# Performance work log

Hardware: AMD Instinct MI355X
Metric: run time of the kernel (lower is better)

Reference implementation:

```python
import jax, jax.numpy as jnp
import numpy as np

N, D_IN, D_HID, D_CODE, K = 131072, 768, 512, 256, 512

def setup_inputs() -> dict:
    key = jax.random.key(0)
    ks = jax.random.split(key, 10)
    s1 = 1.0 / np.sqrt(D_IN); s2 = 1.0 / np.sqrt(D_HID); s3 = 1.0 / np.sqrt(D_CODE)
    return {
        "x": jax.random.normal(ks[0], (N, D_IN), jnp.float32),
        "W1": jax.random.normal(ks[1], (D_IN, D_HID), jnp.float32) * s1,
        "b1": jnp.zeros((D_HID,), jnp.float32),
        "W2": jax.random.normal(ks[2], (D_HID, D_CODE), jnp.float32) * s2,
        "b2": jnp.zeros((D_CODE,), jnp.float32),
        "codebook": jax.random.normal(ks[3], (K, D_CODE), jnp.float32),
        "W3": jax.random.normal(ks[4], (D_CODE, D_HID), jnp.float32) * s3,
        "b3": jnp.zeros((D_HID,), jnp.float32),
        "W4": jax.random.normal(ks[5], (D_HID, D_IN), jnp.float32) * s2,
        "b4": jnp.zeros((D_IN,), jnp.float32),
    }

def reference(x, W1, b1, W2, b2, codebook, W3, b3, W4, b4):
    # encoder: Linear -> ReLU -> Linear
    z = jax.nn.relu(x @ W1 + b1) @ W2 + b2                      # [N, D_CODE]
    # nearest-code search: squared euclidean distances to codebook
    # ||z||^2 - 2 z.c + ||c||^2  (||z||^2 constant per row, drop for argmin)
    dots = z @ codebook.T                                        # [N, K]
    dist = jnp.sum(codebook * codebook, axis=-1)[None, :] - 2.0 * dots
    indices = jnp.argmin(dist, axis=-1)                          # [N] int
    quantized = codebook[indices]                                # gather [N, D_CODE]
    # commitment loss: mse(quantize.detach(), z) * commitment_weight(=1.0)
    commit_loss = jnp.mean((jax.lax.stop_gradient(quantized) - z) ** 2)
    # straight-through estimator
    quantized_st = z + jax.lax.stop_gradient(quantized - z)
    # decoder: Linear -> ReLU -> Linear
    recon = jax.nn.relu(quantized_st @ W3 + b3) @ W4 + b4        # [N, D_IN]
    return recon, indices.astype(jnp.int32), commit_loss
```

## Files before the change

kernel.cpp:

```cpp
#include <hip/hip_runtime.h>
#include <hip/hip_bf16.h>
#include <math.h>

#define N_ROWS 131072
#define DIN    768
#define DHID   512
#define DCODE  256
#define KC     512
#define NFUSE  768
#define TAU1   0.6f
#define TAU2   5e-3f
#define CAP    16384

typedef short short8 __attribute__((ext_vector_type(8)));
typedef float f32x4  __attribute__((ext_vector_type(4)));
typedef unsigned int   u32;
typedef unsigned short u16;

__device__ __forceinline__ void gload16(const void* g, void* l) {
    __builtin_amdgcn_global_load_lds(
        (const __attribute__((address_space(1))) u32*)g,
        (__attribute__((address_space(3))) u32*)l, 16, 0, 0);
}

__device__ __forceinline__ u16 f2bf(float f) {
    u32 u = __builtin_bit_cast(u32, f);
    return (u16)((u + 0x7fffu + ((u >> 16) & 1u)) >> 16);
}
__device__ __forceinline__ float bf2f(u16 h) {
    u32 u = ((u32)h) << 16;
    return __builtin_bit_cast(float, u);
}

__device__ __forceinline__ void xcd_swizzle(int& bxs, int& bys) {
    const int GX  = gridDim.x;
    const int nwg = GX * gridDim.y;
    const int lid = blockIdx.y * GX + blockIdx.x;
    const int chunk = nwg >> 3;
    const int nlid  = (lid & 7) * chunk + (lid >> 3);
    bxs = nlid % GX;
    bys = nlid / GX;
}

__device__ __forceinline__ void split_write(char* hidst, char* lodst, float4 v) {
    u16 h0 = f2bf(v.x), h1 = f2bf(v.y), h2 = f2bf(v.z), h3 = f2bf(v.w);
    u16 l0 = f2bf(__fsub_rn(v.x, bf2f(h0)));
    u16 l1 = f2bf(__fsub_rn(v.y, bf2f(h1)));
    u16 l2 = f2bf(__fsub_rn(v.z, bf2f(h2)));
    u16 l3 = f2bf(__fsub_rn(v.w, bf2f(h3)));
    ushort4 hi; hi.x = h0; hi.y = h1; hi.z = h2; hi.w = h3;
    ushort4 lo; lo.x = l0; lo.y = l1; lo.z = l2; lo.w = l3;
    *(ushort4*)hidst = hi;
    *(ushort4*)lodst = lo;
}

template<int EPI>
__global__ __launch_bounds__(256, 3)
void split2_gemm(const float* __restrict__ Af32,
                 const u16* __restrict__ Ahi, const u16* __restrict__ Alo,
                 const u16* __restrict__ Bhi, const u16* __restrict__ Blo,
                 const float* __restrict__ bias,
                 const float* __restrict__ cnorm,
                 u16* __restrict__ Chi, u16* __restrict__ Clo,
                 float* __restrict__ pd1, int* __restrict__ pi1,
                 float* __restrict__ pd2,
                 int M, int N, int K)
{
    __shared__ char lds[32768];
    const int t = threadIdx.x, lane = t & 63, wid = t >> 6;
    const int wm = wid >> 1, wn = wid & 1;
    int bxs, bys; xcd_swizzle(bxs, bys);
    const int bm = bys * 128, bn = bxs * 128;

    const int sr = lane >> 3, qq = lane & 7, sl = qq ^ sr;
    const u16* bsrc[4];
    #pragma unroll
    for (int c = 0; c < 4; c++) {
        int row = bn + (wid * 4 + c) * 8 + sr;
        const u16* base = (sl < 4) ? Bhi : Blo;
        bsrc[c] = base + (size_t)row * K + (sl & 3) * 8;
    }
    const u16* asrc[4];
    const float* a32src[4];
    int adhi[4], adlo[4];
    if constexpr (EPI == 1) {
        #pragma unroll
        for (int c = 0; c < 4; c++) {
            int row = bm + (wid * 4 + c) * 8 + sr;
            const u16* base = (sl < 4) ? Ahi : Alo;
            asrc[c] = base + (size_t)row * K + (sl & 3) * 8;
        }
    } else {
        #pragma unroll
        for (int c = 0; c < 4; c++) {
            int id = c * 256 + t;
            int row = id >> 3, k4 = id & 7;
            a32src[c] = Af32 + (size_t)(bm + row) * K + k4 * 4;
            int s = k4 >> 1, hf = k4 & 1;
            adhi[c] = row * 128 + ((s ^ (row & 7)) << 4) + hf * 8;
            adlo[c] = row * 128 + (((s | 4) ^ (row & 7)) << 4) + hf * 8;
        }
    }

    f32x4 acc[4][4];
    #pragma unroll
    for (int i = 0; i < 4; i++)
        #pragma unroll
        for (int j = 0; j < 4; j++) acc[i][j] = (f32x4)0.f;

    const int fr = lane & 15, sw = lane & 7;
    const int offhi = (((lane >> 4) ^ sw) << 4);
    const int offlo = ((((lane >> 4) | 4) ^ sw) << 4);
    const int arow = wm * 64 + fr, brow = wn * 64 + fr;
    const int NT = K >> 5;

    for (int tt = 0; tt < NT; tt++) {
        __syncthreads();
        const int kadv = tt * 32;
        #pragma unroll
        for (int c = 0; c < 4; c++)
            gload16(bsrc[c] + kadv, lds + 16384 + (wid * 4 + c) * 1024);
        if constexpr (EPI == 1) {
            #pragma unroll
            for (int c = 0; c < 4; c++)
                gload16(asrc[c] + kadv, lds + (wid * 4 + c) * 1024);
        } else {
            #pragma unroll
            for (int c = 0; c < 4; c++) {
                float4 v = *(const float4*)(a32src[c] + kadv);
                split_write(lds + adhi[c], lds + adlo[c], v);
            }
        }
        __syncthreads();
        char* ab  = lds;
        char* bb2 = lds + 16384;
        short8 ah[4], al[4];
        #pragma unroll
        for (int i = 0; i < 4; i++) {
            ah[i] = *(const short8*)(ab + ((arow + i * 16) << 7) + offhi);
            al[i] = *(const short8*)(ab + ((arow + i * 16) << 7) + offlo);
        }
        #pragma unroll
        for (int j = 0; j < 4; j++) {
            short8 bh = *(const short8*)(bb2 + ((brow + j * 16) << 7) + offhi);
            short8 bl = *(const short8*)(bb2 + ((brow + j * 16) << 7) + offlo);
            #pragma unroll
            for (int i = 0; i < 4; i++) {
                acc[i][j] = __builtin_amdgcn_mfma_f32_16x16x32_bf16(ah[i], bh, acc[i][j], 0, 0, 0);
                acc[i][j] = __builtin_amdgcn_mfma_f32_16x16x32_bf16(al[i], bh, acc[i][j], 0, 0, 0);
                acc[i][j] = __builtin_amdgcn_mfma_f32_16x16x32_bf16(ah[i], bl, acc[i][j], 0, 0, 0);
            }
        }
    }

    if constexpr (EPI == 1) {
        const int ec = lane & 15, g = lane >> 4;
        float cnv[4], bcv[4];
        #pragma unroll
        for (int j = 0; j < 4; j++) {
            int c = bn + wn * 64 + j * 16 + ec;
            cnv[j] = cnorm[c]; bcv[j] = bias[c];
        }
        const int strip = bxs * 2 + wn;
        #pragma unroll
        for (int i = 0; i < 4; i++) {
            #pragma unroll
            for (int e = 0; e < 4; e++) {
                float d1 = INFINITY, d2 = INFINITY; int i1 = 0x7fffffff;
                #pragma unroll
                for (int j = 0; j < 4; j++) {
                    int c = bn + wn * 64 + j * 16 + ec;
                    float d = __fsub_rn(cnv[j],
                              __fmul_rn(2.0f, __fadd_rn(acc[i][j][e], bcv[j])));
                    if (d < d1 || (d == d1 && c < i1)) { d2 = d1; d1 = d; i1 = c; }
                    else if (d < d2) d2 = d;
                }
                #pragma unroll
                for (int m = 1; m < 16; m <<= 1) {
                    float od1 = __shfl_xor(d1, m);
                    int   oi1 = __shfl_xor(i1, m);
                    float od2 = __shfl_xor(d2, m);
                    if (od1 < d1 || (od1 == d1 && oi1 < i1)) {
                        d2 = fminf(d1, od2); d1 = od1; i1 = oi1;
                    } else d2 = fminf(d2, od1);
                }
                if (ec == 0) {
                    int r = bm + wm * 64 + i * 16 + g * 4 + e;
                    pd1[(size_t)strip * M + r] = d1;
                    pi1[(size_t)strip * M + r] = i1;
                    pd2[(size_t)strip * M + r] = d2;
                }
            }
        }
        return;
    } else {
        const int er = (lane >> 4) * 4, ec = lane & 15;
        #pragma unroll
        for (int j = 0; j < 4; j++) {
            int col = bn + wn * 64 + j * 16 + ec;
            float bb = bias[col];
            #pragma unroll
            for (int i = 0; i < 4; i++) {
                #pragma unroll
                for (int e = 0; e < 4; e++) {
                    int r = bm + wm * 64 + i * 16 + er + e;
                    float v = fmaxf(__fadd_rn(acc[i][j][e], bb), 0.f);
                    u16 hi = f2bf(v);
                    u16 lo = f2bf(__fsub_rn(v, bf2f(hi)));
                    Chi[(size_t)r * N + col] = hi;
                    Clo[(size_t)r * N + col] = lo;
                }
            }
        }
    }
}

__global__ __launch_bounds__(256, 3)
void dots_gemm(const u16* __restrict__ A, const u16* __restrict__ BT,
               const float* __restrict__ bias, const float* __restrict__ cnorm,
               float* __restrict__ pd1, int* __restrict__ pi1,
               float* __restrict__ pd2, float* __restrict__ pzn,
               int M, int N, int K)
{
    __shared__ char lds[32768];
    const int t = threadIdx.x, lane = t & 63, wid = t >> 6;
    const int wm = wid >> 1, wn = wid & 1;
    int bxs, bys; xcd_swizzle(bxs, bys);
    const int bm = bys * 128, bn = bxs * 128;

    const int sr = lane >> 3;
    const int sc = ((lane & 7) ^ sr) * 8;
    const u16* aptr[4];
    const u16* bptr[4];
    #pragma unroll
    for (int c = 0; c < 4; c++) {
        int gc = wid * 4 + c;
        aptr[c] = A  + (size_t)(bm + 8 * gc + sr) * K + sc;
        bptr[c] = BT + (size_t)(bn + 8 * gc + sr) * K + sc;
    }

    f32x4 acc[4][4];
    #pragma unroll
    for (int i = 0; i < 4; i++)
        #pragma unroll
        for (int j = 0; j < 4; j++) acc[i][j] = (f32x4)0.f;

    const int koff0 = (16 * (lane >> 4))      ^ ((lane & 7) << 4);
    const int koff1 = (64 + 16 * (lane >> 4)) ^ ((lane & 7) << 4);
    const int arow_rd = wm * 64 + (lane & 15);
    const int brow_rd = wn * 64 + (lane & 15);

    const int NT = K >> 6;
    for (int tt = 0; tt < NT; tt++) {
        __syncthreads();
        const int k0 = tt << 6;
        #pragma unroll
        for (int c = 0; c < 4; c++) {
            int gc = wid * 4 + c;
            gload16(aptr[c] + k0, lds + gc * 1024);
            gload16(bptr[c] + k0, lds + 16384 + gc * 1024);
        }
        __syncthreads();
        char* ldsA = lds;
        char* ldsB = lds + 16384;
        #pragma unroll
        for (int kk = 0; kk < 2; kk++) {
            const int ko = kk ? koff1 : koff0;
            short8 af[4], bfr[4];
            #pragma unroll
            for (int i = 0; i < 4; i++)
                af[i]  = *(const short8*)(ldsA + (arow_rd + i * 16) * 128 + ko);
            #pragma unroll
            for (int j = 0; j < 4; j++)
                bfr[j] = *(const short8*)(ldsB + (brow_rd + j * 16) * 128 + ko);
            #pragma unroll
            for (int i = 0; i < 4; i++)
                #pragma unroll
                for (int j = 0; j < 4; j++)
                    acc[i][j] = __builtin_amdgcn_mfma_f32_16x16x32_bf16(
                        af[i], bfr[j], acc[i][j], 0, 0, 0);
        }
    }

    const int ec = lane & 15, g = lane >> 4;
    if (bxs < 4) {
        float cnv[4], bcv[4];
        #pragma unroll
        for (int j = 0; j < 4; j++) {
            int c = bn + wn * 64 + j * 16 + ec;
            cnv[j] = cnorm[c]; bcv[j] = bias[c];
        }
        const int strip = bxs * 2 + wn;
        #pragma unroll
        for (int i = 0; i < 4; i++) {
            #pragma unroll
            for (int e = 0; e < 4; e++) {
                float d1 = INFINITY, d2 = INFINITY; int i1 = 0x7fffffff;
                #pragma unroll
                for (int j = 0; j < 4; j++) {
                    int c = bn + wn * 64 + j * 16 + ec;
                    float d = __fsub_rn(cnv[j],
                              __fmul_rn(2.0f, __fadd_rn(acc[i][j][e], bcv[j])));
                    if (d < d1 || (d == d1 && c < i1)) { d2 = d1; d1 = d; i1 = c; }
                    else if (d < d2) d2 = d;
                }
                #pragma unroll
                for (int m = 1; m < 16; m <<= 1) {
                    float od1 = __shfl_xor(d1, m);
                    int   oi1 = __shfl_xor(i1, m);
                    float od2 = __shfl_xor(d2, m);
                    if (od1 < d1 || (od1 == d1 && oi1 < i1)) {
                        d2 = fminf(d1, od2); d1 = od1; i1 = oi1;
                    } else d2 = fminf(d2, od1);
                }
                if (ec == 0) {
                    int r = bm + wm * 64 + i * 16 + g * 4 + e;
                    pd1[(size_t)strip * M + r] = d1;
                    pi1[(size_t)strip * M + r] = i1;
                    pd2[(size_t)strip * M + r] = d2;
                }
            }
        }
    } else {
        float bcv[4];
        #pragma unroll
        for (int j = 0; j < 4; j++)
            bcv[j] = bias[bn + wn * 64 + j * 16 + ec];
        const int zs = (bxs - 4) * 2 + wn;
        #pragma unroll
        for (int i = 0; i < 4; i++) {
            #pragma unroll
            for (int e = 0; e < 4; e++) {
                float s = 0.f;
                #pragma unroll
                for (int j = 0; j < 4; j++) {
                    float zv = acc[i][j][e] + bcv[j];
                    s = fmaf(zv, zv, s);
                }
                #pragma unroll
                for (int m = 1; m < 16; m <<= 1) s += __shfl_xor(s, m);
                if (ec == 0) {
                    int r = bm + wm * 64 + i * 16 + g * 4 + e;
                    pzn[(size_t)zs * M + r] = s;
                }
            }
        }
    }
}

template<bool RELU, bool OUT_BF16>
__global__ __launch_bounds__(256, 3)
void mfma_gemm(const u16* __restrict__ A, const u16* __restrict__ BT,
               const float* __restrict__ bias,
               void* __restrict__ Cout, int M, int N, int K)
{
    __shared__ char lds[32768];
    const int t    = threadIdx.x;
    const int lane = t & 63, wid = t >> 6;
    const int wm   = wid >> 1, wn = wid & 1;
    int bxs, bys;
    xcd_swizzle(bxs, bys);
    const int bm = bys * 128, bn = bxs * 128;

    const int sr = lane >> 3;
    const int sc = ((lane & 7) ^ sr) * 8;
    const u16* aptr[4];
    const u16* bptr[4];
    #pragma unroll
    for (int c = 0; c < 4; c++) {
        int gc   = wid * 4 + c;
        aptr[c] = A  + (size_t)(bm + 8 * gc + sr) * K + sc;
        bptr[c] = BT + (size_t)(bn + 8 * gc + sr) * K + sc;
    }

    f32x4 acc[4][4];
    #pragma unroll
    for (int i = 0; i < 4; i++)
        #pragma unroll
        for (int j = 0; j < 4; j++) acc[i][j] = (f32x4)0.f;

    const int koff0 = (16 * (lane >> 4))      ^ ((lane & 7) << 4);
    const int koff1 = (64 + 16 * (lane >> 4)) ^ ((lane & 7) << 4);
    const int arow_rd = wm * 64 + (lane & 15);
    const int brow_rd = wn * 64 + (lane & 15);

    const int NT = K >> 6;
    for (int tt = 0; tt < NT; tt++) {
        __syncthreads();
        const int k0 = tt << 6;
        #pragma unroll
        for (int c = 0; c < 4; c++) {
            int gc = wid * 4 + c;
            gload16(aptr[c] + k0, lds + gc * 1024);
            gload16(bptr[c] + k0, lds + 16384 + gc * 1024);
        }
        __syncthreads();
        char* ldsA = lds;
        char* ldsB = lds + 16384;
        #pragma unroll
        for (int kk = 0; kk < 2; kk++) {
            const int ko = kk ? koff1 : koff0;
            short8 af[4], bfr[4];
            #pragma unroll
            for (int i = 0; i < 4; i++)
                af[i]  = *(const short8*)(ldsA + (arow_rd + i * 16) * 128 + ko);
            #pragma unroll
            for (int j = 0; j < 4; j++)
                bfr[j] = *(const short8*)(ldsB + (brow_rd + j * 16) * 128 + ko);
            #pragma unroll
            for (int i = 0; i < 4; i++)
                #pragma unroll
                for (int j = 0; j < 4; j++)
                    acc[i][j] = __builtin_amdgcn_mfma_f32_16x16x32_bf16(
                        af[i], bfr[j], acc[i][j], 0, 0, 0);
        }
    }

    const int er = (lane >> 4) * 4;
    const int ec = lane & 15;
    #pragma unroll
    for (int j = 0; j < 4; j++) {
        int col  = bn + wn * 64 + j * 16 + ec;
        float bb = bias[col];
        #pragma unroll
        for (int i = 0; i < 4; i++) {
            #pragma unroll
            for (int e = 0; e < 4; e++) {
                int r   = bm + wm * 64 + i * 16 + er + e;
                float v = acc[i][j][e] + bb;
                if (RELU) v = fmaxf(v, 0.f);
                if (OUT_BF16) ((u16*)Cout)[(size_t)r * N + col]  = f2bf(v);
                else          ((float*)Cout)[(size_t)r * N + col] = v;
            }
        }
    }
}

__global__ __launch_bounds__(256)
void gather_out(const float* __restrict__ R, const int* __restrict__ idxi,
                float* __restrict__ out)
{
    int w    = (blockIdx.x * 256 + threadIdx.x) >> 6;
    int lane = threadIdx.x & 63;
    int nw   = (gridDim.x * 256) >> 6;
    for (int r = w; r < N_ROWS; r += nw) {
        int code = idxi[r];
        const float4* src = (const float4*)(R + (size_t)code * DIN);
        float4* dst = (float4*)(out + (size_t)r * DIN);
        dst[lane]       = src[lane];
        dst[lane + 64]  = src[lane + 64];
        dst[lane + 128] = src[lane + 128];
    }
}

__global__ void transpose_cb_kernel(const float* __restrict__ cb, float* __restrict__ cbT)
{
    int tid = blockIdx.x * 256 + threadIdx.x;
    int k = tid >> 8;
    int d = tid & 255;
    cbT[(size_t)d * KC + k] = cb[(size_t)k * DCODE + d];
}

__global__ void cast_bf16_kernel(const float* __restrict__ in, u16* __restrict__ out, int n)
{
    int i = blockIdx.x * 256 + threadIdx.x;
    if (i < n) out[i] = f2bf(in[i]);
}

__global__ void castT_bf16_kernel(const float* __restrict__ in, u16* __restrict__ out,
                                  int K, int N)
{
    int i = blockIdx.x * 256 + threadIdx.x;
    if (i >= K * N) return;
    int n = i / K, k = i - n * K;
    out[i] = f2bf(in[(size_t)k * N + n]);
}

__global__ void prep_W1T(const float* __restrict__ W1, u16* __restrict__ Thi,
                         u16* __restrict__ Tlo)
{
    int id = blockIdx.x * 256 + threadIdx.x;
    if (id >= DHID * DIN) return;
    int n = id / DIN, k = id - n * DIN;
    float v = W1[(size_t)k * DHID + n];
    u16 hi = f2bf(v);
    Thi[id] = hi;
    Tlo[id] = f2bf(__fsub_rn(v, bf2f(hi)));
}

__global__ void prep_Wc(const float* __restrict__ W2, const float* __restrict__ cb,
                        u16* __restrict__ Thi, u16* __restrict__ Tlo)
{
    int id = blockIdx.x * 256 + threadIdx.x;
    int n = id & 511, h = id >> 9;
    double acc = 0.0;
    for (int tt2 = 0; tt2 < DCODE; tt2++)
        acc += (double)W2[(size_t)h * DCODE + tt2] * (double)cb[(size_t)n * DCODE + tt2];
    float v = (float)acc;
    u16 hi = f2bf(v);
    Thi[(size_t)n * DHID + h] = hi;
    Tlo[(size_t)n * DHID + h] = f2bf(__fsub_rn(v, bf2f(hi)));
}

__global__ void prep_W2T(const float* __restrict__ W2, u16* __restrict__ T)
{
    int id = blockIdx.x * 256 + threadIdx.x;
    if (id >= DCODE * DHID) return;
    int t2 = id >> 9, h = id & 511;
    T[(size_t)(KC + t2) * DHID + h] = f2bf(W2[(size_t)h * DCODE + t2]);
}

__global__ void prep_bcf(const float* __restrict__ b2, const float* __restrict__ cb,
                         float* __restrict__ bcf)
{
    int n = blockIdx.x * 256 + threadIdx.x;
    if (n >= NFUSE) return;
    if (n < KC) {
        double acc = 0.0;
        for (int tt2 = 0; tt2 < DCODE; tt2++)
            acc += (double)b2[tt2] * (double)cb[(size_t)n * DCODE + tt2];
        bcf[n] = (float)acc;
    } else {
        bcf[n] = b2[n - KC];
    }
}

__global__ void cnorm_np_kernel(const float* __restrict__ cb, float* __restrict__ cnorm)
{
    int k = blockIdx.x * 64 + threadIdx.x;
    if (k >= KC) return;
    const float* c = cb + (size_t)k * DCODE;
    float bsum[2];
    #pragma unroll
    for (int b = 0; b < 2; b++) {
        const float* a = c + b * 128;
        float r[8];
        #pragma unroll
        for (int j = 0; j < 8; j++) r[j] = __fmul_rn(a[j], a[j]);
        for (int i = 8; i < 128; i += 8)
            #pragma unroll
            for (int j = 0; j < 8; j++)
                r[j] = __fadd_rn(r[j], __fmul_rn(a[i + j], a[i + j]));
        bsum[b] = __fadd_rn(
            __fadd_rn(__fadd_rn(r[0], r[1]), __fadd_rn(r[2], r[3])),
            __fadd_rn(__fadd_rn(r[4], r[5]), __fadd_rn(r[6], r[7])));
    }
    cnorm[k] = __fadd_rn(bsum[0], bsum[1]);
}

__global__ void final_argmin_flag(const float* __restrict__ pd1,
                                  const int* __restrict__ pi1,
                                  const float* __restrict__ pd2,
                                  const float* __restrict__ pzn,
                                  float* __restrict__ idx_f,
                                  int* __restrict__ idx_i,
                                  float* __restrict__ rowloss,
                                  int* __restrict__ cnt,
                                  int* __restrict__ list)
{
    int r = blockIdx.x * 256 + threadIdx.x;
    if (r >= N_ROWS) return;
    float d1 = pd1[r]; int i1 = pi1[r]; float d2 = pd2[r];
    #pragma unroll
    for (int b = 1; b < 8; b++) {
        float od1 = pd1[(size_t)b * N_ROWS + r];
        int   oi1 = pi1[(size_t)b * N_ROWS + r];
        float od2 = pd2[(size_t)b * N_ROWS + r];
        if (od1 < d1 || (od1 == d1 && oi1 < i1)) {
            d2 = fminf(d1, od2); d1 = od1; i1 = oi1;
        } else d2 = fminf(d2, od1);
    }
    float zn = pzn[r] + pzn[(size_t)N_ROWS + r]
             + pzn[(size_t)2 * N_ROWS + r] + pzn[(size_t)3 * N_ROWS + r];
    idx_f[r]   = (float)i1;
    idx_i[r]   = i1;
    rowloss[r] = zn + d1;
    if (d2 - d1 < TAU1) {
        int p = atomicAdd(cnt, 1);
        list[p] = r;
    }
}

__global__ void gather_h1(const u16* __restrict__ h1hi, const u16* __restrict__ h1lo,
                          const int* __restrict__ list, const int* __restrict__ cnt,
                          u16* __restrict__ ghi, u16* __restrict__ glo)
{
    int n1 = *cnt; if (n1 > CAP) n1 = CAP;
    int total = n1 * 64;
    for (int c = blockIdx.x * blockDim.x + threadIdx.x; c < total;
         c += gridDim.x * blockDim.x) {
        int i = c >> 6, o = (c & 63) * 8;
        int row = list[i];
        *(short8*)(ghi + (size_t)i * DHID + o) =
            *(const short8*)(h1hi + (size_t)row * DHID + o);
        *(short8*)(glo + (size_t)i * DHID + o) =
            *(const short8*)(h1lo + (size_t)row * DHID + o);
    }
}

__global__ void merge2_flag(const float* __restrict__ pd1b,
                            const int* __restrict__ pi1b,
                            const float* __restrict__ pd2b,
                            const int* __restrict__ list,
                            const int* __restrict__ cnt1,
                            float* __restrict__ idx_f, int* __restrict__ idx_i,
                            int* __restrict__ cnt2, int* __restrict__ list2)
{
    int i = blockIdx.x * 256 + threadIdx.x;
    if (i >= CAP) return;
    int n1 = *cnt1; if (n1 > CAP) n1 = CAP;
    if (i >= n1) return;
    float d1 = pd1b[i]; int i1 = pi1b[i]; float d2 = pd2b[i];
    #pragma unroll
    for (int b = 1; b < 8; b++) {
        float od1 = pd1b[(size_t)b * CAP + i];
        int   oi1 = pi1b[(size_t)b * CAP + i];
        float od2 = pd2b[(size_t)b * CAP + i];
        if (od1 < d1 || (od1 == d1 && oi1 < i1)) {
            d2 = fminf(d1, od2); d1 = od1; i1 = oi1;
        } else d2 = fminf(d2, od1);
    }
    int row = list[i];
    idx_f[row] = (float)i1;
    idx_i[row] = i1;
    if (d2 - d1 < TAU2) {
        int p = atomicAdd(cnt2, 1);
        list2[p] = row;
    }
}

__global__ void overflow_append(const int* __restrict__ list,
                                const int* __restrict__ cnt1,
                                int* __restrict__ cnt2, int* __restrict__ list2)
{
    int i = CAP + blockIdx.x * 256 + threadIdx.x;
    if (i < *cnt1) {
        int p = atomicAdd(cnt2, 1);
        list2[p] = list[i];
    }
}

__global__ __launch_bounds__(512)
void recompute_kernel(const float* __restrict__ x,  const float* __restrict__ W1,
                      const float* __restrict__ b1, const float* __restrict__ W2,
                      const float* __restrict__ b2, const float* __restrict__ cbT,
                      const float* __restrict__ cnorm,
                      const int* __restrict__ cnt,  const int* __restrict__ list,
                      float* __restrict__ idx_f,    int* __restrict__ idx_i)
{
    __shared__ float xs[8][DIN];
    __shared__ float h1s[8][DHID];
    __shared__ float zs[8][DCODE];
    __shared__ float swd[8][8];
    __shared__ int   swi[8][8];
    __shared__ int   rls[8];
    const int t = threadIdx.x;
    const int n = *cnt;

    for (int base = blockIdx.x * 8; base < n; base += gridDim.x * 8) {
        __syncthreads();
        if (t < 8) rls[t] = (base + t < n) ? list[base + t] : -1;
        __syncthreads();
        #pragma unroll
        for (int rr = 0; rr < 8; rr++) {
            int row = rls[rr];
            if (row >= 0)
                for (int i = t; i < DIN; i += 512)
                    xs[rr][i] = x[(size_t)row * DIN + i];
        }
        __syncthreads();
        {
            float acc[8] = {0.f,0.f,0.f,0.f,0.f,0.f,0.f,0.f};
            for (int i = 0; i < DIN; i++) {
                float w = W1[(size_t)i * DHID + t];
                #pragma unroll
                for (int rr = 0; rr < 8; rr++)
                    acc[rr] = fmaf(xs[rr][i], w, acc[rr]);
            }
            float bb = b1[t];
            #pragma unroll
            for (int rr = 0; rr < 8; rr++)
                h1s[rr][t] = fmaxf(__fadd_rn(acc[rr], bb), 0.f);
        }
        __syncthreads();
        {
            int half = t >> 8, t2 = t & 255;
            float acc[4] = {0.f,0.f,0.f,0.f};
            for (int h = 0; h < DHID; h++) {
                float w = W2[(size_t)h * DCODE + t2];
                #pragma unroll
                for (int q2 = 0; q2 < 4; q2++)
                    acc[q2] = fmaf(h1s[half * 4 + q2][h], w, acc[q2]);
            }
            float bb = b2[t2];
            #pragma unroll
            for (int q2 = 0; q2 < 4; q2++)
                zs[half * 4 + q2][t2] = __fadd_rn(acc[q2], bb);
        }
        __syncthreads();
        {
            float acc[8] = {0.f,0.f,0.f,0.f,0.f,0.f,0.f,0.f};
            for (int d = 0; d < DCODE; d++) {
                float c = cbT[(size_t)d * KC + t];
                #pragma unroll
                for (int rr = 0; rr < 8; rr++)
                    acc[rr] = fmaf(zs[rr][d], c, acc[rr]);
            }
            float cn = cnorm[t];
            #pragma unroll
            for (int rr = 0; rr < 8; rr++) {
                float d = __fsub_rn(cn, __fmul_rn(2.0f, acc[rr]));
                int ii = t;
                #pragma unroll
                for (int m = 1; m < 64; m <<= 1) {
                    float od = __shfl_xor(d, m);
                    int   oi = __shfl_xor(ii, m);
                    if (od < d || (od == d && oi < ii)) { d = od; ii = oi; }
                }
                if ((t & 63) == 0) { swd[rr][t >> 6] = d; swi[rr][t >> 6] = ii; }
            }
        }
        __syncthreads();
        if (t < 8) {
            int row = rls[t];
            if (row >= 0) {
                float d = swd[t][0]; int ii = swi[t][0];
                #pragma unroll
                for (int w = 1; w < 8; w++) {
                    float od = swd[t][w]; int oi = swi[t][w];
                    if (od < d || (od == d && oi < ii)) { d = od; ii = oi; }
                }
                idx_i[row] = ii;
                idx_f[row] = (float)ii;
            }
        }
    }
}

__global__ void loss_reduce_kernel(const float* __restrict__ rowloss,
                                   double* __restrict__ acc, int n)
{
    double s = 0.0;
    for (int i = blockIdx.x * blockDim.x + threadIdx.x; i < n; i += gridDim.x * blockDim.x)
        s += (double)rowloss[i];
    for (int off = 32; off; off >>= 1) s += __shfl_xor(s, off);
    __shared__ double red[4];
    int lane = threadIdx.x & 63, wave = threadIdx.x >> 6;
    if (lane == 0) red[wave] = s;
    __syncthreads();
    if (threadIdx.x == 0) {
        double b = red[0] + red[1] + red[2] + red[3];
        atomicAdd(acc, b);
    }
}

__global__ void finalize_kernel(const double* __restrict__ acc, float* __restrict__ out)
{
    out[0] = (float)(acc[0] / ((double)N_ROWS * (double)DCODE));
}

extern "C" void kernel_launch(void* const* d_in, const int* in_sizes, int n_in,
                              void* d_out, int out_size, void* d_ws, size_t ws_size,
                              hipStream_t stream)
{
    const float* x  = (const float*)d_in[0];
    const float* W1 = (const float*)d_in[1];
    const float* b1 = (const float*)d_in[2];
    const float* W2 = (const float*)d_in[3];
    const float* b2 = (const float*)d_in[4];
    const float* cb = (const float*)d_in[5];
    const float* W3 = (const float*)d_in[6];
    const float* b3 = (const float*)d_in[7];
    const float* W4 = (const float*)d_in[8];
    const float* b4 = (const float*)d_in[9];
    float* out = (float*)d_out;
    char*  ws  = (char*)d_ws;

    u16*    h1hi    = (u16*)   (ws);
    u16*    h1lo    = (u16*)   (ws + 134217728);
    float*  pd1     = (float*) (ws + 268435456);
    int*    pi1     = (int*)   (ws + 272629760);
    float*  pd2     = (float*) (ws + 276824064);
    float*  pzn     = (float*) (ws + 281018368);
    float*  pd1b    = (float*) (ws + 283115520);
    int*    pi1b    = (int*)   (ws + 283639808);
    float*  pd2b    = (float*) (ws + 284164096);
    u16*    h1ghi   = (u16*)   (ws + 284688384);
    u16*    h1glo   = (u16*)   (ws + 301465600);
    float*  rowloss = (float*) (ws + 318242816);
    int*    idxi    = (int*)   (ws + 318767104);
    int*    list    = (int*)   (ws + 319291392);
    int*    list2   = (int*)   (ws + 319815680);
    int*    rcnt1   = (int*)   (ws + 320339968);
    int*    rcnt2   = (int*)   (ws + 320339972);
    double* lossa   = (double*)(ws + 320340032);
    u16*    W1Thi   = (u16*)   (ws + 320340096);
    u16*    W1Tlo   = (u16*)   (ws + 321126528);
    u16*    Wfb     = (u16*)   (ws + 321912960);
    u16*    WfTlo   = (u16*)   (ws + 322699392);
    u16*    cbB     = (u16*)   (ws + 323223680);
    u16*    W3T     = (u16*)   (ws + 323485824);
    u16*    W4T     = (u16*)   (ws + 323747968);
    float*  bcf     = (float*) (ws + 324534400);
    float*  cnorm   = (float*) (ws + 324537472);
    float*  cbT     = (float*) (ws + 324539520);
    u16*    R1b     = (u16*)   (ws + 325063808);
    float*  Rf      = (float*) (ws + 325588096);

    float* idxf    = out + (size_t)N_ROWS * DIN;
    float* lossout = idxf + N_ROWS;

    hipMemsetAsync(ws + 320339968, 0, 128, stream);

    transpose_cb_kernel<<<512, 256, 0, stream>>>(cb, cbT);
    cnorm_np_kernel<<<8, 64, 0, stream>>>(cb, cnorm);
    cast_bf16_kernel<<<(KC*DCODE)/256, 256, 0, stream>>>(cb, cbB, KC*DCODE);
    castT_bf16_kernel<<<(DCODE*DHID)/256, 256, 0, stream>>>(W3, W3T, DCODE, DHID);
    castT_bf16_kernel<<<(DHID*DIN)/256, 256, 0, stream>>>(W4, W4T, DHID, DIN);
    prep_W1T<<<(DHID*DIN)/256, 256, 0, stream>>>(W1, W1Thi, W1Tlo);
    prep_Wc<<<(KC*DHID)/256, 256, 0, stream>>>(W2, cb, Wfb, WfTlo);
    prep_W2T<<<(DCODE*DHID)/256, 256, 0, stream>>>(W2, Wfb);
    prep_bcf<<<3, 256, 0, stream>>>(b2, cb, bcf);

    mfma_gemm<true,  true ><<<dim3(4, 4), 256, 0, stream>>>(
        cbB, W3T, b3, (void*)R1b, KC, DHID, DCODE);
    mfma_gemm<false, false><<<dim3(6, 4), 256, 0, stream>>>(
        R1b, W4T, b4, (void*)Rf, KC, DIN, DHID);

    split2_gemm<0><<<dim3(DHID/128, N_ROWS/128), 256, 0, stream>>>(
        x, nullptr, nullptr, W1Thi, W1Tlo, b1, nullptr,
        h1hi, h1lo, nullptr, nullptr, nullptr, N_ROWS, DHID, DIN);
    dots_gemm<<<dim3(NFUSE/128, N_ROWS/128), 256, 0, stream>>>(
        h1hi, Wfb, bcf, cnorm, pd1, pi1, pd2, pzn, N_ROWS, NFUSE, DHID);
    final_argmin_flag<<<N_ROWS/256, 256, 0, stream>>>(
        pd1, pi1, pd2, pzn, idxf, idxi, rowloss, rcnt1, list);

    gather_h1<<<512, 256, 0, stream>>>(h1hi, h1lo, list, rcnt1, h1ghi, h1glo);
    split2_gemm<1><<<dim3(KC/128, CAP/128), 256, 0, stream>>>(
        nullptr, h1ghi, h1glo, Wfb, WfTlo, bcf, cnorm,
        nullptr, nullptr, pd1b, pi1b, pd2b, CAP, KC, DHID);
    merge2_flag<<<CAP/256, 256, 0, stream>>>(
        pd1b, pi1b, pd2b, list, rcnt1, idxf, idxi, rcnt2, list2);
    overflow_append<<<(N_ROWS-CAP)/256, 256, 0, stream>>>(list, rcnt1, rcnt2, list2);

    recompute_kernel<<<2048, 512, 0, stream>>>(
        x, W1, b1, W2, b2, cbT, cnorm, rcnt2, list2, idxf, idxi);

    gather_out<<<4096, 256, 0, stream>>>(Rf, idxi, out);

    loss_reduce_kernel<<<256, 256, 0, stream>>>(rowloss, lossa, N_ROWS);
    finalize_kernel<<<1, 1, 0, stream>>>(lossa, lossout);
}
```

Measured before the change: 879.5 us.

## Compute first layer in plain bf16, recompute split-precision only for ambiguous rows

```diff
diff --git a/kernel.cpp b/kernel.cpp
--- a/kernel.cpp
+++ b/kernel.cpp
@@ -8,9 +8,9 @@
 #define DCODE  256
 #define KC     512
 #define NFUSE  768
-#define TAU1   0.6f
+#define TAU1   1.5f
 #define TAU2   5e-3f
-#define CAP    16384
+#define CAP    32768
 
 typedef short short8 __attribute__((ext_vector_type(8)));
 typedef float f32x4  __attribute__((ext_vector_type(4)));
@@ -52,6 +52,103 @@
     ushort4 lo; lo.x = l0; lo.y = l1; lo.z = l2; lo.w = l3;
     *(ushort4*)hidst = hi;
     *(ushort4*)lodst = lo;
+}
+
+__global__ __launch_bounds__(256, 3)
+void h1_plain(const float* __restrict__ x, const u16* __restrict__ W1T,
+              const float* __restrict__ b1, u16* __restrict__ h1b,
+              int M, int N, int K)
+{
+    __shared__ char lds[32768];
+    const int t = threadIdx.x, lane = t & 63, wid = t >> 6;
+    const int wm = wid >> 1, wn = wid & 1;
+    int bxs, bys; xcd_swizzle(bxs, bys);
+    const int bm = bys * 128, bn = bxs * 128;
+
+    const int sr = lane >> 3;
+    const int sc = ((lane & 7) ^ sr) * 8;
+    const u16* bptr[4];
+    #pragma unroll
+    for (int c = 0; c < 4; c++) {
+        int brow = bn + 8 * (wid * 4 + c) + sr;
+        bptr[c] = W1T + (size_t)brow * K + sc;
+    }
+    const float* asrc[4];
+    int albyte[4];
+    #pragma unroll
+    for (int c = 0; c < 4; c++) {
+        int id = c * 256 + t;
+        int row = id >> 3, g = id & 7;
+        asrc[c]   = x + (size_t)(bm + row) * K + g * 8;
+        albyte[c] = row * 128 + ((g ^ (row & 7)) << 4);
+    }
+
+    f32x4 acc[4][4];
+    #pragma unroll
+    for (int i = 0; i < 4; i++)
+        #pragma unroll
+        for (int j = 0; j < 4; j++) acc[i][j] = (f32x4)0.f;
+
+    const int koff0 = (16 * (lane >> 4))      ^ ((lane & 7) << 4);
+    const int koff1 = (64 + 16 * (lane >> 4)) ^ ((lane & 7) << 4);
+    const int arow_rd = wm * 64 + (lane & 15);
+    const int brow_rd = wn * 64 + (lane & 15);
+
+    const int NT = K >> 6;
+    for (int tt = 0; tt < NT; tt++) {
+        __syncthreads();
+        const int k0 = tt << 6;
+        #pragma unroll
+        for (int c = 0; c < 4; c++)
+            gload16(bptr[c] + k0, lds + 16384 + (wid * 4 + c) * 1024);
+        #pragma unroll
+        for (int c = 0; c < 4; c++) {
+            float4 v0 = *(const float4*)(asrc[c] + k0);
+            float4 v1 = *(const float4*)(asrc[c] + k0 + 4);
+            short8 p;
+            p[0] = (short)f2bf(v0.x); p[1] = (short)f2bf(v0.y);
+            p[2] = (short)f2bf(v0.z); p[3] = (short)f2bf(v0.w);
+            p[4] = (short)f2bf(v1.x); p[5] = (short)f2bf(v1.y);
+            p[6] = (short)f2bf(v1.z); p[7] = (short)f2bf(v1.w);
+            *(short8*)(lds + albyte[c]) = p;
+        }
+        __syncthreads();
+        char* ldsA = lds;
+        char* ldsB = lds + 16384;
+        #pragma unroll
+        for (int kk = 0; kk < 2; kk++) {
+            const int ko = kk ? koff1 : koff0;
+            short8 af[4], bfr[4];
+            #pragma unroll
+            for (int i = 0; i < 4; i++)
+                af[i]  = *(const short8*)(ldsA + (arow_rd + i * 16) * 128 + ko);
+            #pragma unroll
+            for (int j = 0; j < 4; j++)
+                bfr[j] = *(const short8*)(ldsB + (brow_rd + j * 16) * 128 + ko);
+            #pragma unroll
+            for (int i = 0; i < 4; i++)
+                #pragma unroll
+                for (int j = 0; j < 4; j++)
+                    acc[i][j] = __builtin_amdgcn_mfma_f32_16x16x32_bf16(
+                        af[i], bfr[j], acc[i][j], 0, 0, 0);
+        }
+    }
+
+    const int er = (lane >> 4) * 4, ec = lane & 15;
+    #pragma unroll
+    for (int j = 0; j < 4; j++) {
+        int col  = bn + wn * 64 + j * 16 + ec;
+        float bb = b1[col];
+        #pragma unroll
+        for (int i = 0; i < 4; i++) {
+            #pragma unroll
+            for (int e = 0; e < 4; e++) {
+                int r   = bm + wm * 64 + i * 16 + er + e;
+                float v = fmaxf(acc[i][j][e] + bb, 0.f);
+                h1b[(size_t)r * N + col] = f2bf(v);
+            }
+        }
+    }
 }
 
 template<int EPI>
@@ -453,6 +550,24 @@
     }
 }
 
+__global__ __launch_bounds__(256)
+void gather_x(const float* __restrict__ x, const int* __restrict__ list,
+              const int* __restrict__ cnt, float* __restrict__ xg)
+{
+    int n1 = *cnt; if (n1 > CAP) n1 = CAP;
+    int w    = (blockIdx.x * 256 + threadIdx.x) >> 6;
+    int lane = threadIdx.x & 63;
+    int nw   = (gridDim.x * 256) >> 6;
+    for (int i = w; i < n1; i += nw) {
+        int row = list[i];
+        const float4* src = (const float4*)(x + (size_t)row * DIN);
+        float4* dst = (float4*)(xg + (size_t)i * DIN);
+        dst[lane]       = src[lane];
+        dst[lane + 64]  = src[lane + 64];
+        dst[lane + 128] = src[lane + 128];
+    }
+}
+
 __global__ void transpose_cb_kernel(const float* __restrict__ cb, float* __restrict__ cbT)
 {
     int tid = blockIdx.x * 256 + threadIdx.x;
@@ -578,23 +693,6 @@
     if (d2 - d1 < TAU1) {
         int p = atomicAdd(cnt, 1);
         list[p] = r;
-    }
-}
-
-__global__ void gather_h1(const u16* __restrict__ h1hi, const u16* __restrict__ h1lo,
-                          const int* __restrict__ list, const int* __restrict__ cnt,
-                          u16* __restrict__ ghi, u16* __restrict__ glo)
-{
-    int n1 = *cnt; if (n1 > CAP) n1 = CAP;
-    int total = n1 * 64;
-    for (int c = blockIdx.x * blockDim.x + threadIdx.x; c < total;
-         c += gridDim.x * blockDim.x) {
-        int i = c >> 6, o = (c & 63) * 8;
-        int row = list[i];
-        *(short8*)(ghi + (size_t)i * DHID + o) =
-            *(const short8*)(h1hi + (size_t)row * DHID + o);
-        *(short8*)(glo + (size_t)i * DHID + o) =
-            *(const short8*)(h1lo + (size_t)row * DHID + o);
     }
 }
 
@@ -776,41 +874,41 @@
     float* out = (float*)d_out;
     char*  ws  = (char*)d_ws;
 
-    u16*    h1hi    = (u16*)   (ws);
-    u16*    h1lo    = (u16*)   (ws + 134217728);
-    float*  pd1     = (float*) (ws + 268435456);
-    int*    pi1     = (int*)   (ws + 272629760);
-    float*  pd2     = (float*) (ws + 276824064);
-    float*  pzn     = (float*) (ws + 281018368);
-    float*  pd1b    = (float*) (ws + 283115520);
-    int*    pi1b    = (int*)   (ws + 283639808);
-    float*  pd2b    = (float*) (ws + 284164096);
-    u16*    h1ghi   = (u16*)   (ws + 284688384);
-    u16*    h1glo   = (u16*)   (ws + 301465600);
-    float*  rowloss = (float*) (ws + 318242816);
-    int*    idxi    = (int*)   (ws + 318767104);
-    int*    list    = (int*)   (ws + 319291392);
-    int*    list2   = (int*)   (ws + 319815680);
-    int*    rcnt1   = (int*)   (ws + 320339968);
-    int*    rcnt2   = (int*)   (ws + 320339972);
-    double* lossa   = (double*)(ws + 320340032);
-    u16*    W1Thi   = (u16*)   (ws + 320340096);
-    u16*    W1Tlo   = (u16*)   (ws + 321126528);
-    u16*    Wfb     = (u16*)   (ws + 321912960);
-    u16*    WfTlo   = (u16*)   (ws + 322699392);
-    u16*    cbB     = (u16*)   (ws + 323223680);
-    u16*    W3T     = (u16*)   (ws + 323485824);
-    u16*    W4T     = (u16*)   (ws + 323747968);
-    float*  bcf     = (float*) (ws + 324534400);
-    float*  cnorm   = (float*) (ws + 324537472);
-    float*  cbT     = (float*) (ws + 324539520);
-    u16*    R1b     = (u16*)   (ws + 325063808);
-    float*  Rf      = (float*) (ws + 325588096);
+    u16*    h1b     = (u16*)   (ws);
+    float*  pd1     = (float*) (ws + 134217728);
+    int*    pi1     = (int*)   (ws + 138412032);
+    float*  pd2     = (float*) (ws + 142606336);
+    float*  pzn     = (float*) (ws + 146800640);
+    float*  pd1b    = (float*) (ws + 148897792);
+    int*    pi1b    = (int*)   (ws + 149946368);
+    float*  pd2b    = (float*) (ws + 150994944);
+    float*  xg      = (float*) (ws + 152043520);
+    u16*    h1ghi   = (u16*)   (ws + 252706816);
+    u16*    h1glo   = (u16*)   (ws + 286261248);
+    float*  rowloss = (float*) (ws + 319815680);
+    int*    idxi    = (int*)   (ws + 320339968);
+    int*    list    = (int*)   (ws + 320864256);
+    int*    list2   = (int*)   (ws + 321388544);
+    int*    rcnt1   = (int*)   (ws + 321912832);
+    int*    rcnt2   = (int*)   (ws + 321912836);
+    double* lossa   = (double*)(ws + 321912896);
+    u16*    W1Thi   = (u16*)   (ws + 321912960);
+    u16*    W1Tlo   = (u16*)   (ws + 322699392);
+    u16*    Wfb     = (u16*)   (ws + 323485824);
+    u16*    WfTlo   = (u16*)   (ws + 324272256);
+    u16*    cbB     = (u16*)   (ws + 324796544);
+    u16*    W3T     = (u16*)   (ws + 325058688);
+    u16*    W4T     = (u16*)   (ws + 325320832);
+    float*  bcf     = (float*) (ws + 326107264);
+    float*  cnorm   = (float*) (ws + 326110336);
+    float*  cbT     = (float*) (ws + 326112384);
+    u16*    R1b     = (u16*)   (ws + 326636672);
+    float*  Rf      = (float*) (ws + 327160960);
 
     float* idxf    = out + (size_t)N_ROWS * DIN;
     float* lossout = idxf + N_ROWS;
 
-    hipMemsetAsync(ws + 320339968, 0, 128, stream);
+    hipMemsetAsync(ws + 321912832, 0, 128, stream);
 
     transpose_cb_kernel<<<512, 256, 0, stream>>>(cb, cbT);
     cnorm_np_kernel<<<8, 64, 0, stream>>>(cb, cnorm);
@@ -827,15 +925,17 @@
     mfma_gemm<false, false><<<dim3(6, 4), 256, 0, stream>>>(
         R1b, W4T, b4, (void*)Rf, KC, DIN, DHID);
 
-    split2_gemm<0><<<dim3(DHID/128, N_ROWS/128), 256, 0, stream>>>(
-        x, nullptr, nullptr, W1Thi, W1Tlo, b1, nullptr,
-        h1hi, h1lo, nullptr, nullptr, nullptr, N_ROWS, DHID, DIN);
+    h1_plain<<<dim3(DHID/128, N_ROWS/128), 256, 0, stream>>>(
+        x, W1Thi, b1, h1b, N_ROWS, DHID, DIN);
     dots_gemm<<<dim3(NFUSE/128, N_ROWS/128), 256, 0, stream>>>(
-        h1hi, Wfb, bcf, cnorm, pd1, pi1, pd2, pzn, N_ROWS, NFUSE, DHID);
+        h1b, Wfb, bcf, cnorm, pd1, pi1, pd2, pzn, N_ROWS, NFUSE, DHID);
     final_argmin_flag<<<N_ROWS/256, 256, 0, stream>>>(
         pd1, pi1, pd2, pzn, idxf, idxi, rowloss, rcnt1, list);
 
-    gather_h1<<<512, 256, 0, stream>>>(h1hi, h1lo, list, rcnt1, h1ghi, h1glo);
+    gather_x<<<2048, 256, 0, stream>>>(x, list, rcnt1, xg);
+    split2_gemm<0><<<dim3(DHID/128, CAP/128), 256, 0, stream>>>(
+        xg, nullptr, nullptr, W1Thi, W1Tlo, b1, nullptr,
+        h1ghi, h1glo, nullptr, nullptr, nullptr, CAP, DHID, DIN);
     split2_gemm<1><<<dim3(KC/128, CAP/128), 256, 0, stream>>>(
         nullptr, h1ghi, h1glo, Wfb, WfTlo, bcf, cnorm,
         nullptr, nullptr, pd1b, pi1b, pd2b, CAP, KC, DHID);
```

After: 885.1 us. Within noise of the previous version (+0.6%).
